# Performance work log

Measured on AMD Instinct MI355X. Metric: run time of the kernel, lower is better.

The kernel has to match this reference:

```python
import jax, jax.numpy as jnp
import numpy as np

D = 1024
H = 16
HD = D // H
LN_EPS = 1e-5
RMS_EPS = 1e-6


def layernorm(x, g, b):
    mu = jnp.mean(x, axis=-1, keepdims=True)
    var = jnp.mean(jnp.square(x - mu), axis=-1, keepdims=True)
    return (x - mu) * jax.lax.rsqrt(var + LN_EPS) * g + b


def rmsnorm(x, w):
    ms = jnp.mean(jnp.square(x), axis=-1, keepdims=True)
    return x * jax.lax.rsqrt(ms + RMS_EPS) * w


def setup_inputs() -> dict:
    key = jax.random.key(0)
    ks = jax.random.split(key, 8)
    s = 0.02
    ones = jnp.ones((D,), jnp.float32)
    zeros = jnp.zeros((D,), jnp.float32)
    return {
        "query_tokens": jax.random.normal(ks[0], (4, 512, D), jnp.float32),
        "point_features": jax.random.normal(ks[1], (4, 4096, D), jnp.float32),
        "ln_q_g": ones, "ln_q_b": zeros,
        "ln_kv_g": ones, "ln_kv_b": zeros,
        "Wq": jax.random.normal(ks[2], (D, D), jnp.float32) * s, "bq": zeros,
        "Wk": jax.random.normal(ks[3], (D, D), jnp.float32) * s, "bk": zeros,
        "Wv": jax.random.normal(ks[4], (D, D), jnp.float32) * s, "bv": zeros,
        "rms_q_w": ones, "rms_k_w": ones,
        "Wo": jax.random.normal(ks[5], (D, D), jnp.float32) * s, "bo": zeros,
        "ln_mlp_g": ones, "ln_mlp_b": zeros,
        "W1": jax.random.normal(ks[6], (D, 4 * D), jnp.float32) * s,
        "b1": jnp.zeros((4 * D,), jnp.float32),
        "W2": jax.random.normal(ks[7], (4 * D, D), jnp.float32) * s,
        "b2": zeros,
    }


def reference(query_tokens, point_features, ln_q_g, ln_q_b, ln_kv_g, ln_kv_b,
              Wq, bq, Wk, bk, Wv, bv, rms_q_w, rms_k_w, Wo, bo,
              ln_mlp_g, ln_mlp_b, W1, b1, W2, b2):
    B, K, _ = query_tokens.shape
    N = point_features.shape[1]
    q_in = layernorm(query_tokens, ln_q_g, ln_q_b)
    kv_in = layernorm(point_features, ln_kv_g, ln_kv_b)
    q = rmsnorm(q_in @ Wq + bq, rms_q_w)          # [B,K,D]
    k = rmsnorm(kv_in @ Wk + bk, rms_k_w)         # [B,N,D]
    v = kv_in @ Wv + bv                            # [B,N,D]
    q = q.reshape(B, K, H, HD)
    k = k.reshape(B, N, H, HD)
    v = v.reshape(B, N, H, HD)
    scores = jnp.einsum('bkhd,bnhd->bhkn', q, k) / jnp.sqrt(jnp.float32(HD))
    attn = jax.nn.softmax(scores, axis=-1)
    ctx = jnp.einsum('bhkn,bnhd->bkhd', attn, v).reshape(B, K, D)
    out = ctx @ Wo + bo + query_tokens
    h = layernorm(out, ln_mlp_g, ln_mlp_b)
    mlp = jax.nn.gelu(h @ W1 + b1, approximate=False) @ W2 + b2
    return out + mlp
```

## Files before the change

kernel.cpp:

```cpp
#include <hip/hip_runtime.h>
#include <math.h>

#define DD   1024
#define NHD  16
#define HDIM 64
#define BB   4
#define QN   512
#define KVN  4096
#define FF   4096

typedef __attribute__((ext_vector_type(8))) short bf16x8;
typedef __attribute__((ext_vector_type(4))) float f32x4;

__device__ __forceinline__ float b2f(ushort u){
  union { unsigned u32; float f; } x; x.u32 = ((unsigned)u)<<16; return x.f;
}
__device__ __forceinline__ ushort f2b(float f){
  unsigned u = __float_as_uint(f);
  unsigned r = (u + 0x7FFFu + ((u>>16)&1u)) >> 16;
  return (ushort)r;
}
__device__ __forceinline__ float ldx(const void* p, size_t i, int isbf){
  return isbf ? b2f(((const ushort*)p)[i]) : ((const float*)p)[i];
}
__device__ __forceinline__ int detect_bf(const void* gref){
  return ((const unsigned*)gref)[0] == 0x3F803F80u;
}

#if defined(__has_builtin)
#if __has_builtin(__builtin_amdgcn_global_load_lds)
#define HAS_GLL 1
#endif
#endif
#ifndef HAS_GLL
#define HAS_GLL 0
#endif
__device__ __forceinline__ void stage16(const ushort* g, ushort* lds_base, int lane){
#if HAS_GLL
  __builtin_amdgcn_global_load_lds(g, lds_base, 16, 0, 0);
#else
  *(uint4*)(lds_base + lane*8) = *(const uint4*)g;
#endif
}

__device__ __forceinline__ void wave_barrier(){
  asm volatile("" ::: "memory");
  __builtin_amdgcn_s_barrier();
  asm volatile("" ::: "memory");
}

__global__ __launch_bounds__(256)
void trans_all(const void* __restrict__ Wq, const void* __restrict__ Wk,
               const void* __restrict__ Wv, const void* __restrict__ Wo,
               const void* __restrict__ W1, const void* __restrict__ W2,
               ushort* __restrict__ WqT, ushort* __restrict__ WkvT,
               ushort* __restrict__ WoT,
               ushort* __restrict__ W1T, ushort* __restrict__ W2T,
               const void* __restrict__ gref)
{
  const int isbf = detect_bf(gref);
  int bid = blockIdx.x;
  const void* src; ushort* dst; int R, C, tid;
  if (bid < 1024){
    int s = bid >> 8; tid = bid & 255; R = 1024; C = 1024;
    src = (s==0) ? Wq : (s==1) ? Wk : (s==2) ? Wv : Wo;
    dst = (s==0) ? WqT : (s==1) ? WkvT : (s==2) ? (WkvT + (size_t)1024*1024) : WoT;
  } else if (bid < 2048){ tid = bid - 1024; src = W1; dst = W1T; R = 1024; C = 4096; }
  else                  { tid = bid - 2048; src = W2; dst = W2T; R = 4096; C = 1024; }
  int ntx = C >> 6;
  int tx = tid % ntx, ty = tid / ntx;
  int r0 = ty*64, c0 = tx*64;

  __shared__ __align__(16) ushort tile[64][72];
  int t = threadIdx.x;
  if (isbf){
    #pragma unroll
    for (int i=0;i<2;i++){
      int idx = t + i*256;
      int r = idx>>3, ch = idx&7;
      #pragma unroll
      for (int j=0;j<8;j++)
        tile[r][ch*8+j] = ((const ushort*)src)[(size_t)(r0+r)*C + c0 + ch*8 + j];
    }
  } else {
    #pragma unroll
    for (int i=0;i<2;i++){
      int idx = t + i*256;
      int r = idx>>3, ch = idx&7;
      const float* s4 = (const float*)src + (size_t)(r0+r)*C + c0 + ch*8;
      float4 f0 = *(const float4*)s4;
      float4 f1 = *(const float4*)(s4+4);
      tile[r][ch*8+0]=f2b(f0.x); tile[r][ch*8+1]=f2b(f0.y);
      tile[r][ch*8+2]=f2b(f0.z); tile[r][ch*8+3]=f2b(f0.w);
      tile[r][ch*8+4]=f2b(f1.x); tile[r][ch*8+5]=f2b(f1.y);
      tile[r][ch*8+6]=f2b(f1.z); tile[r][ch*8+7]=f2b(f1.w);
    }
  }
  __syncthreads();
  #pragma unroll
  for (int i=0;i<2;i++){
    int idx = t + i*256;
    int c = idx>>3, ch = idx&7;
    __align__(16) ushort tmp[8];
    #pragma unroll
    for (int j=0;j<8;j++) tmp[j] = tile[ch*8+j][c];
    *(uint4*)(dst + (size_t)(c0+c)*R + r0 + ch*8) = *(uint4*)tmp;
  }
}

__global__ __launch_bounds__(256)
void ln_all(const void* __restrict__ qtok, const void* __restrict__ pfeat,
            const void* __restrict__ gq, const void* __restrict__ bq,
            const void* __restrict__ gkv, const void* __restrict__ bkv,
            ushort* __restrict__ q_ln, ushort* __restrict__ kv_ln,
            const void* __restrict__ gref)
{
  const int isbf = detect_bf(gref);
  int row = blockIdx.x, t = threadIdx.x;
  const void* src; const void* g; const void* bb; ushort* dst; int r;
  if (row < BB*QN){ src = qtok;  g = gq;  bb = bq;  dst = q_ln;  r = row; }
  else            { src = pfeat; g = gkv; bb = bkv; dst = kv_ln; r = row - BB*QN; }
  int c0 = t*4;
  float v[4];
  if (isbf){
    #pragma unroll
    for (int i=0;i<4;i++) v[i] = b2f(((const ushort*)src)[(size_t)r*DD + c0 + i]);
  } else {
    float4 f = *(const float4*)((const float*)src + (size_t)r*DD + c0);
    v[0]=f.x; v[1]=f.y; v[2]=f.z; v[3]=f.w;
  }
  float s1=0.f, s2=0.f;
  #pragma unroll
  for (int i=0;i<4;i++){ s1 += v[i]; s2 += v[i]*v[i]; }
  #pragma unroll
  for (int off=32; off; off>>=1){ s1 += __shfl_xor(s1,off,64); s2 += __shfl_xor(s2,off,64); }
  __shared__ float r1[4], r2[4];
  int wave = t>>6;
  if ((t&63)==0){ r1[wave]=s1; r2[wave]=s2; }
  __syncthreads();
  s1 = r1[0]+r1[1]+r1[2]+r1[3];
  s2 = r2[0]+r2[1]+r2[2]+r2[3];
  float mu  = s1 * (1.0f/DD);
  float var = s2 * (1.0f/DD) - mu*mu;
  float rs  = rsqrtf(var + 1e-5f);
  union { ushort u[4]; uint2 w; } pk;
  #pragma unroll
  for (int i=0;i<4;i++)
    pk.u[i] = f2b((v[i]-mu)*rs*ldx(g,c0+i,isbf) + ldx(bb,c0+i,isbf));
  *(uint2*)(dst + (size_t)r*DD + c0) = pk.w;
}

__global__ __launch_bounds__(256)
void ln_f32(const float* __restrict__ x, const void* __restrict__ g,
            const void* __restrict__ bb, ushort* __restrict__ y,
            const void* __restrict__ gref)
{
  const int isbf = detect_bf(gref);
  int row = blockIdx.x, t = threadIdx.x;
  int c0 = t*4;
  float4 f = *(const float4*)(x + (size_t)row*DD + c0);
  float v[4] = {f.x, f.y, f.z, f.w};
  float s1=0.f, s2=0.f;
  #pragma unroll
  for (int i=0;i<4;i++){ s1 += v[i]; s2 += v[i]*v[i]; }
  #pragma unroll
  for (int off=32; off; off>>=1){ s1 += __shfl_xor(s1,off,64); s2 += __shfl_xor(s2,off,64); }
  __shared__ float r1[4], r2[4];
  int wave = t>>6;
  if ((t&63)==0){ r1[wave]=s1; r2[wave]=s2; }
  __syncthreads();
  s1 = r1[0]+r1[1]+r1[2]+r1[3];
  s2 = r2[0]+r2[1]+r2[2]+r2[3];
  float mu  = s1 * (1.0f/DD);
  float var = s2 * (1.0f/DD) - mu*mu;
  float rs  = rsqrtf(var + 1e-5f);
  union { ushort u[4]; uint2 w; } pk;
  #pragma unroll
  for (int i=0;i<4;i++)
    pk.u[i] = f2b((v[i]-mu)*rs*ldx(g,c0+i,isbf) + ldx(bb,c0+i,isbf));
  *(uint2*)(y + (size_t)row*DD + c0) = pk.w;
}

__global__ __launch_bounds__(256)
void rms_all(ushort* __restrict__ qb, const void* __restrict__ wq,
             ushort* __restrict__ kb, const void* __restrict__ wk,
             const void* __restrict__ gref)
{
  const int isbf = detect_bf(gref);
  int row = blockIdx.x, t = threadIdx.x;
  ushort* x; const void* w; int r;
  if (row < BB*QN){ x = qb; w = wq; r = row; }
  else            { x = kb; w = wk; r = row - BB*QN; }
  int c0 = t*4;
  union { ushort u[4]; uint2 w; } in;
  in.w = *(const uint2*)(x + (size_t)r*DD + c0);
  float v[4];
  #pragma unroll
  for (int i=0;i<4;i++) v[i] = b2f(in.u[i]);
  float s2 = 0.f;
  #pragma unroll
  for (int i=0;i<4;i++) s2 += v[i]*v[i];
  #pragma unroll
  for (int off=32; off; off>>=1) s2 += __shfl_xor(s2,off,64);
  __shared__ float r2[4];
  int wave = t>>6;
  if ((t&63)==0) r2[wave]=s2;
  __syncthreads();
  s2 = r2[0]+r2[1]+r2[2]+r2[3];
  float rs = rsqrtf(s2*(1.0f/DD) + 1e-6f);
  union { ushort u[4]; uint2 w; } pk;
  #pragma unroll
  for (int i=0;i<4;i++) pk.u[i] = f2b(v[i]*rs*ldx(w,c0+i,isbf));
  *(uint2*)(x + (size_t)r*DD + c0) = pk.w;
}

template<int ACT_GELU, int OUT_MODE, int RES_MODE>
__global__ __launch_bounds__(256)
void gemm_bt(const ushort* __restrict__ A, const ushort* __restrict__ BT,
             const void* __restrict__ bias,
             const void* __restrict__ res_ext, const float* __restrict__ res_f,
             void* __restrict__ Cout, void* __restrict__ Cout2,
             int M, int N, int Kdim,
             const void* __restrict__ gref)
{
  const int isbf = detect_bf(gref);
  __shared__ __align__(16) ushort As[128*64];
  __shared__ __align__(16) ushort Bs[128*64];
  const int bm = blockIdx.y * 128;
  const int bn = blockIdx.x * 128;
  const int t = threadIdx.x;
  const int wave = t>>6, lane = t&63, quad = lane>>4, l16 = lane&15;
  const int wm = (wave&1)*64, wn = (wave>>1)*64;

  const ushort* ga[4]; const ushort* gb[4];
  #pragma unroll
  for (int j=0;j<4;j++){
    int row = (t>>3) + j*32;
    int g = ((t&7) - row) & 7;
    ga[j] = A  + (size_t)(bm+row)*Kdim + g*8;
    gb[j] = BT + (size_t)(bn+row)*Kdim + g*8;
  }

  int offA[2][4], offB[2][4];
  #pragma unroll
  for (int kk=0;kk<2;kk++)
    #pragma unroll
    for (int i=0;i<4;i++){
      int ra = wm + i*16 + l16;
      offA[kk][i] = ra*64 + ((quad + kk*4 + ra)&7)*8;
      int rb = wn + i*16 + l16;
      offB[kk][i] = rb*64 + ((quad + kk*4 + rb)&7)*8;
    }

  f32x4 zero = {0.f,0.f,0.f,0.f};
  f32x4 acc[4][4];
  #pragma unroll
  for (int i=0;i<4;i++)
    #pragma unroll
    for (int j=0;j<4;j++) acc[i][j] = zero;

  const int kiters = Kdim >> 6;
  for (int ki = 0; ki < kiters; ki++) {
    #pragma unroll
    for (int j=0;j<4;j++){
      stage16(ga[j], As + (size_t)(j*256 + wave*64)*8, lane);
      stage16(gb[j], Bs + (size_t)(j*256 + wave*64)*8, lane);
      ga[j] += 64; gb[j] += 64;
    }
    __syncthreads();
    #pragma unroll
    for (int kk=0;kk<2;kk++){
      bf16x8 af[4], bfr[4];
      #pragma unroll
      for (int i=0;i<4;i++){
        af[i]  = *(const bf16x8*)(As + offA[kk][i]);
        bfr[i] = *(const bf16x8*)(Bs + offB[kk][i]);
      }
      #pragma unroll
      for (int mt=0;mt<4;mt++)
        #pragma unroll
        for (int nt=0;nt<4;nt++)
          acc[mt][nt] = __builtin_amdgcn_mfma_f32_16x16x32_bf16(af[mt], bfr[nt], acc[mt][nt], 0,0,0);
    }
    __syncthreads();
  }

  if (OUT_MODE == 3){
    if (bn < 1024){
      float bv[4];
      #pragma unroll
      for (int nt=0;nt<4;nt++) bv[nt] = ldx(bias, bn + wn + nt*16 + l16, isbf);
      ushort* kout = (ushort*)Cout;
      #pragma unroll
      for (int mt=0;mt<4;mt++){
        #pragma unroll
        for (int r=0;r<4;r++){
          int row = bm + wm + mt*16 + quad*4 + r;
          #pragma unroll
          for (int nt=0;nt<4;nt++){
            int col = bn + wn + nt*16 + l16;
            kout[(size_t)row*1024 + col] = f2b(acc[mt][nt][r] + bv[nt]);
          }
        }
      }
    } else {
      float bv[4];
      #pragma unroll
      for (int nt=0;nt<4;nt++) bv[nt] = ldx(res_ext, bn-1024 + wn + nt*16 + l16, isbf);
      ushort* Vt = (ushort*)Cout2;
      #pragma unroll
      for (int mt=0;mt<4;mt++){
        int row0 = bm + wm + mt*16 + quad*4;
        int b = row0 >> 12, tok = row0 & (KVN-1);
        #pragma unroll
        for (int nt=0;nt<4;nt++){
          int cl = bn-1024 + wn + nt*16 + l16;
          union { ushort u[4]; uint2 w; } pk;
          #pragma unroll
          for (int r=0;r<4;r++) pk.u[r] = f2b(acc[mt][nt][r] + bv[nt]);
          size_t o = ((size_t)((b*NHD + (cl>>6))*HDIM + (cl&63)))*KVN + tok;
          *(uint2*)(Vt + o) = pk.w;
        }
      }
    }
    return;
  }

  float bv[4];
  #pragma unroll
  for (int nt=0;nt<4;nt++) bv[nt] = ldx(bias, bn + wn + nt*16 + l16, isbf);
  #pragma unroll
  for (int mt=0;mt<4;mt++){
    #pragma unroll
    for (int r=0;r<4;r++){
      int row = bm + wm + mt*16 + quad*4 + r;
      #pragma unroll
      for (int nt=0;nt<4;nt++){
        int col = bn + wn + nt*16 + l16;
        float v = acc[mt][nt][r] + bv[nt];
        if (ACT_GELU) v = 0.5f*v*(1.0f + erff(v*0.70710678118f));
        size_t oi = (size_t)row*N + col;
        if (RES_MODE==1) v += ldx(res_ext, oi, isbf);
        if (RES_MODE==2) v += res_f[oi];
        if (OUT_MODE==0)      ((ushort*)Cout)[oi] = f2b(v);
        else if (OUT_MODE==1) ((float*)Cout)[oi]  = v;
        else { if (isbf) ((ushort*)Cout)[oi] = f2b(v); else ((float*)Cout)[oi] = v; }
      }
    }
  }
}

#define G_HB  32768
#define G_RA0 0
#define G_RA1 8192
#define G_RB0 16384
#define G_RB1 24576

#define G_STAGE(src, R, tile) do{ \
  ushort* _d = ldsb + (((tile)&1)*G_HB + (R) + wave*1024); \
  stage16(src[0] + ((tile)<<6), _d,       lane); \
  stage16(src[1] + ((tile)<<6), _d + 512, lane); \
}while(0)

#define G_LDA(dst, base) \
  _Pragma("unroll") for (int kk=0;kk<2;kk++) \
  _Pragma("unroll") for (int m=0;m<4;m++) \
    dst[kk][m] = *(const bf16x8*)((base) + offA[kk][m]);

#define G_LDB(dst, base) \
  _Pragma("unroll") for (int kk=0;kk<2;kk++) \
  _Pragma("unroll") for (int n=0;n<2;n++) \
    dst[kk][n] = *(const bf16x8*)((base) + offB[kk][n]);

#define G_MM16(ar, br, MO, NO) \
  _Pragma("unroll") for (int kk=0;kk<2;kk++) \
  _Pragma("unroll") for (int m=0;m<4;m++) \
  _Pragma("unroll") for (int n=0;n<2;n++) \
    acc[m+(MO)][n+(NO)] = __builtin_amdgcn_mfma_f32_16x16x32_bf16(ar[kk][m], br[kk][n], acc[m+(MO)][n+(NO)], 0,0,0);

#define G_SYNC() do{ wave_barrier(); \
  asm volatile("s_waitcnt lgkmcnt(0)" ::: "memory"); \
  __builtin_amdgcn_sched_barrier(0); \
  __builtin_amdgcn_s_setprio(1); }while(0)

#define G_END() do{ __builtin_amdgcn_s_setprio(0); wave_barrier(); }while(0)

__global__ __launch_bounds__(512, 2)
void gemm256_kv(const ushort* __restrict__ A, const ushort* __restrict__ BT,
                const void* __restrict__ biasK, const void* __restrict__ biasV,
                ushort* __restrict__ Kout, ushort* __restrict__ Vt,
                int Kdim, const void* __restrict__ gref)
{
  const int isbf = detect_bf(gref);
  __shared__ __align__(16) ushort ldsb[65536];
  const int bm = blockIdx.y * 256;
  const int bn = blockIdx.x * 256;
  const int t = threadIdx.x;
  const int wave = t>>6, lane = t&63, quad = lane>>4, l16 = lane&15;
  const int wg = wave>>2, wn = wave&3;

  const ushort *sA0[2], *sA1[2], *sB0[2], *sB1[2];
  #pragma unroll
  for (int jj=0;jj<2;jj++){
    int r = (wave*2 + jj)*8 + (lane>>3);
    int g = ((lane&7) - r) & 7;
    int grA0 = r + (r & 64);
    int gc0  = (r & 31) + ((r >> 5) << 6);
    sA0[jj] = A  + (size_t)(bm + grA0     )*Kdim + g*8;
    sA1[jj] = A  + (size_t)(bm + grA0 + 64)*Kdim + g*8;
    sB0[jj] = BT + (size_t)(bn + gc0      )*Kdim + g*8;
    sB1[jj] = BT + (size_t)(bn + gc0 + 32 )*Kdim + g*8;
  }

  int offA[2][4], offB[2][2];
  #pragma unroll
  for (int kk=0;kk<2;kk++){
    int slot = ((kk*4 + quad + l16) & 7) * 8;
    #pragma unroll
    for (int m=0;m<4;m++) offA[kk][m] = (wg*64 + m*16 + l16)*64 + slot;
    #pragma unroll
    for (int n=0;n<2;n++) offB[kk][n] = (wn*32 + n*16 + l16)*64 + slot;
  }

  f32x4 zero = {0.f,0.f,0.f,0.f};
  f32x4 acc[8][4];
  #pragma unroll
  for (int i=0;i<8;i++)
    #pragma unroll
    for (int j=0;j<4;j++) acc[i][j] = zero;

  G_STAGE(sA0, G_RA0, 0);
  G_STAGE(sB0, G_RB0, 0);
  G_STAGE(sB1, G_RB1, 0);
  G_STAGE(sA1, G_RA1, 0);
  G_STAGE(sA0, G_RA0, 1);
  G_STAGE(sB1, G_RB1, 1);
  G_STAGE(sA1, G_RA1, 1);
  asm volatile("s_waitcnt vmcnt(6)" ::: "memory");
  wave_barrier();

  const int niter = Kdim >> 7;
  const ushort* L0 = ldsb;
  const ushort* L1 = ldsb + G_HB;
  bf16x8 a[2][4], b[2][2], b1[2][2];

  for (int i = 0; i < niter; ++i) {
    const bool st = (i + 1 < niter);
    G_LDA(a, L0 + G_RA0); G_LDB(b, L0 + G_RB0);
    G_STAGE(sB0, G_RB0, 2*i+1);
    G_SYNC(); G_MM16(a, b, 0, 0); G_END();
    G_LDB(b1, L0 + G_RB1);
    if (st) G_STAGE(sA0, G_RA0, 2*i+2);
    G_SYNC(); G_MM16(a, b1, 0, 2); G_END();
    G_LDA(a, L0 + G_RA1);
    if (st) G_STAGE(sB1, G_RB1, 2*i+2);
    G_SYNC(); G_MM16(a, b1, 4, 2); G_END();
    G_LDB(b, L0 + G_RB0);
    if (st) G_STAGE(sA1, G_RA1, 2*i+2);
    G_SYNC(); G_MM16(a, b, 4, 0);
    __builtin_amdgcn_s_setprio(0);
    if (st) { asm volatile("s_waitcnt vmcnt(6)" ::: "memory"); }
    else    { asm volatile("s_waitcnt vmcnt(0)" ::: "memory"); }
    wave_barrier();
    G_LDA(a, L1 + G_RA0); G_LDB(b, L1 + G_RB0);
    if (st) G_STAGE(sB0, G_RB0, 2*i+2);
    G_SYNC(); G_MM16(a, b, 0, 0); G_END();
    G_LDB(b1, L1 + G_RB1);
    if (st) G_STAGE(sA0, G_RA0, 2*i+3);
    G_SYNC(); G_MM16(a, b1, 0, 2); G_END();
    G_LDA(a, L1 + G_RA1);
    if (st) G_STAGE(sB1, G_RB1, 2*i+3);
    G_SYNC(); G_MM16(a, b1, 4, 2); G_END();
    G_LDB(b, L1 + G_RB0);
    if (st) G_STAGE(sA1, G_RA1, 2*i+3);
    G_SYNC(); G_MM16(a, b, 4, 0);
    __builtin_amdgcn_s_setprio(0);
    if (st) { asm volatile("s_waitcnt vmcnt(6)" ::: "memory"); }
    wave_barrier();
  }

  if (bn < 1024){
    float bvv[4];
    #pragma unroll
    for (int nt=0;nt<4;nt++) bvv[nt] = ldx(biasK, bn + wn*64 + nt*16 + l16, isbf);
    #pragma unroll
    for (int mt=0;mt<8;mt++){
      #pragma unroll
      for (int r=0;r<4;r++){
        int row = bm + wg*128 + mt*16 + quad*4 + r;
        #pragma unroll
        for (int nt=0;nt<4;nt++){
          int col = bn + wn*64 + nt*16 + l16;
          Kout[(size_t)row*1024 + col] = f2b(acc[mt][nt][r] + bvv[nt]);
        }
      }
    }
  } else {
    float bvv[4];
    #pragma unroll
    for (int nt=0;nt<4;nt++) bvv[nt] = ldx(biasV, bn - 1024 + wn*64 + nt*16 + l16, isbf);
    #pragma unroll
    for (int mt=0;mt<8;mt++){
      int row0 = bm + wg*128 + mt*16 + quad*4;
      int bi = row0 >> 12, tok = row0 & (KVN-1);
      #pragma unroll
      for (int nt=0;nt<4;nt++){
        int cl = bn - 1024 + wn*64 + nt*16 + l16;
        union { ushort u[4]; uint2 w2; } pk;
        #pragma unroll
        for (int r=0;r<4;r++) pk.u[r] = f2b(acc[mt][nt][r] + bvv[nt]);
        size_t o = ((size_t)((bi*NHD + (cl>>6))*HDIM + (cl&63)))*KVN + tok;
        *(uint2*)(Vt + o) = pk.w2;
      }
    }
  }
}

__global__ __launch_bounds__(256, 3)
void flash_attn3(const ushort* __restrict__ Q, const ushort* __restrict__ K,
                 const ushort* __restrict__ Vt, float* __restrict__ Op,
                 float* __restrict__ ML)
{
  __shared__ __align__(16) ushort Ks[128*72];
  __shared__ __align__(16) ushort Vs[64*136];
  __shared__ __align__(16) ushort Ps[4][16*136];
  const int bh = blockIdx.x, qt = blockIdx.y, hf = blockIdx.z;
  const int b = bh>>4, h = bh&15;
  const int t = threadIdx.x, wave = t>>6, lane = t&63, quad = lane>>4, l16 = lane&15;
  ushort* Pz = Ps[wave];

  const float QS = 0.125f * 1.4426950408889634f;
  bf16x8 qf[2][2];
  #pragma unroll
  for (int mt=0;mt<2;mt++){
    const ushort* qb = Q + (size_t)(b*QN + qt*128 + wave*32 + mt*16 + l16)*DD + h*HDIM;
    bf16x8 r0 = *(const bf16x8*)(qb + quad*8);
    bf16x8 r1 = *(const bf16x8*)(qb + 32 + quad*8);
    #pragma unroll
    for (int j=0;j<8;j++){
      qf[mt][0][j] = (short)f2b(b2f((ushort)r0[j]) * QS);
      qf[mt][1][j] = (short)f2b(b2f((ushort)r1[j]) * QS);
    }
  }

  f32x4 zero = {0.f,0.f,0.f,0.f};
  f32x4 o[2][4];
  #pragma unroll
  for (int mt=0;mt<2;mt++)
    #pragma unroll
    for (int nt=0;nt<4;nt++) o[mt][nt] = zero;
  float lp[2][4] = {{0.f,0.f,0.f,0.f},{0.f,0.f,0.f,0.f}};

  const ushort* kgb = K  + (size_t)(b*KVN + hf*1024)*DD + h*HDIM;
  const ushort* vtb = Vt + ((size_t)bh*HDIM)*KVN + hf*1024;
  const int kcs = t&7;

  for (int kv0 = 0; kv0 < 1024; kv0 += 128) {
    #pragma unroll
    for (int j=0;j<4;j++){
      int kr = (t>>3) + j*32;
      *(uint4*)(Ks + kr*72 + kcs*8) =
        *(const uint4*)(kgb + (size_t)(kv0+kr)*DD + kcs*8);
    }
    #pragma unroll
    for (int j=0;j<4;j++){
      int p = t + j*256; int vr = p>>4, vc = p&15;
      uint4 d = *(const uint4*)(vtb + (size_t)vr*KVN + kv0 + vc*8);
      ushort* pv = (ushort*)&d;
      ushort* vbp = Vs + vr*136 + (vc&1)*64 + (vc>>1);
      #pragma unroll
      for (int jj=0;jj<8;jj++) vbp[jj*8] = pv[jj];
    }
    __syncthreads();

    f32x4 pb[2][8];
    #pragma unroll
    for (int nt=0;nt<8;nt++){
      const ushort* kb = Ks + (nt*16+l16)*72 + quad*8;
      bf16x8 kf0 = *(const bf16x8*)kb;
      bf16x8 kf1 = *(const bf16x8*)(kb + 32);
      #pragma unroll
      for (int mt=0;mt<2;mt++){
        f32x4 a = __builtin_amdgcn_mfma_f32_16x16x32_bf16(qf[mt][0], kf0, zero, 0,0,0);
        a = __builtin_amdgcn_mfma_f32_16x16x32_bf16(qf[mt][1], kf1, a, 0,0,0);
        #pragma unroll
        for (int r=0;r<4;r++) a[r] = __builtin_amdgcn_exp2f(fminf(a[r], 88.f));
        pb[mt][nt] = a;
      }
    }
    #pragma unroll
    for (int mt=0;mt<2;mt++){
      #pragma unroll
      for (int r=0;r<4;r++){
        float ls = 0.f;
        bf16x8 pk;
        #pragma unroll
        for (int nt=0;nt<8;nt++){
          ls += pb[mt][nt][r];
          pk[nt] = (short)(__float_as_uint(pb[mt][nt][r]) >> 16);
        }
        lp[mt][r] += ls;
        *(bf16x8*)(Pz + (quad*4+r)*136 + l16*8) = pk;
      }
      #pragma unroll
      for (int kc=0;kc<4;kc++){
        bf16x8 pa = *(const bf16x8*)(Pz + l16*136 + kc*32 + quad*8);
        pb[mt][kc] = *(f32x4*)&pa;
      }
    }
    #pragma unroll
    for (int nt=0;nt<4;nt++){
      const ushort* vbr = Vs + (nt*16+l16)*136;
      #pragma unroll
      for (int kc=0;kc<4;kc++){
        bf16x8 vf = *(const bf16x8*)(vbr + kc*32 + quad*8);
        o[0][nt] = __builtin_amdgcn_mfma_f32_16x16x32_bf16(*(bf16x8*)&pb[0][kc], vf, o[0][nt], 0,0,0);
        o[1][nt] = __builtin_amdgcn_mfma_f32_16x16x32_bf16(*(bf16x8*)&pb[1][kc], vf, o[1][nt], 0,0,0);
      }
    }
    __syncthreads();
  }

  const int slot = hf*256 + bh*4 + qt;
  float* Ob = Op + (size_t)slot*128*64;
  #pragma unroll
  for (int mt=0;mt<2;mt++)
    #pragma unroll
    for (int nt=0;nt<4;nt++)
      #pragma unroll
      for (int r=0;r<4;r++)
        Ob[(wave*32 + mt*16 + quad*4 + r)*64 + nt*16 + l16] = o[mt][nt][r];
  #pragma unroll
  for (int mt=0;mt<2;mt++)
    #pragma unroll
    for (int r=0;r<4;r++){
      float v = lp[mt][r];
      #pragma unroll
      for (int off=1; off<16; off<<=1) v += __shfl_xor(v, off, 64);
      if (l16 == 0)
        ML[(size_t)slot*128 + wave*32 + mt*16 + quad*4 + r] = v;
    }
}

__global__ __launch_bounds__(256)
void flash_combine4(const float* __restrict__ Op, const float* __restrict__ ML,
                    ushort* __restrict__ Ctx)
{
  const int bq = blockIdx.x;
  const int bh = bq>>2, qt = bq&3;
  const int b = bh>>4, h = bh&15;
  const int t = threadIdx.x;
  const int row = t>>1, hd0 = (t&1)*32;
  float l = 0.f;
  #pragma unroll
  for (int i=0;i<4;i++) l += ML[(size_t)(i*256 + bq)*128 + row];
  float inv = 1.0f / l;
  float4 a[8];
  #pragma unroll
  for (int c=0;c<8;c++){ a[c].x=0.f; a[c].y=0.f; a[c].z=0.f; a[c].w=0.f; }
  #pragma unroll
  for (int i=0;i<4;i++){
    const float* s = Op + ((size_t)(i*256 + bq)*128 + row)*64 + hd0;
    #pragma unroll
    for (int c=0;c<8;c++){
      float4 v = *(const float4*)(s + c*4);
      a[c].x += v.x; a[c].y += v.y; a[c].z += v.z; a[c].w += v.w;
    }
  }
  ushort* dst = Ctx + (size_t)(b*QN + qt*128 + row)*DD + h*HDIM + hd0;
  #pragma unroll
  for (int c=0;c<8;c++){
    union { ushort u[4]; uint2 w; } pk;
    pk.u[0] = f2b(a[c].x*inv); pk.u[1] = f2b(a[c].y*inv);
    pk.u[2] = f2b(a[c].z*inv); pk.u[3] = f2b(a[c].w*inv);
    *(uint2*)(dst + c*4) = pk.w;
  }
}

extern "C" void kernel_launch(void* const* d_in, const int* in_sizes, int n_in,
                              void* d_out, int out_size, void* d_ws, size_t ws_size,
                              hipStream_t stream)
{
  const void* qtok    = d_in[0];
  const void* pfeat   = d_in[1];
  const void* ln_q_g  = d_in[2];
  const void* ln_q_b  = d_in[3];
  const void* ln_kv_g = d_in[4];
  const void* ln_kv_b = d_in[5];
  const void* Wq      = d_in[6];
  const void* bq      = d_in[7];
  const void* Wk      = d_in[8];
  const void* bk      = d_in[9];
  const void* Wv      = d_in[10];
  const void* bv      = d_in[11];
  const void* rms_q_w = d_in[12];
  const void* rms_k_w = d_in[13];
  const void* Wo      = d_in[14];
  const void* bo      = d_in[15];
  const void* ln_mlp_g= d_in[16];
  const void* ln_mlp_b= d_in[17];
  const void* W1      = d_in[18];
  const void* b1      = d_in[19];
  const void* W2      = d_in[20];
  const void* b2      = d_in[21];
  const void* gref    = ln_q_g;

  char* w = (char*)d_ws;
  auto take = [&](size_t bytes)->char*{ char* p = w; w += (bytes + 255) & ~(size_t)255; return p; };
  ushort* WqT  = (ushort*)take((size_t)DD*DD*2);
  ushort* WkvT = (ushort*)take((size_t)2*DD*DD*2);
  ushort* WoT  = (ushort*)take((size_t)DD*DD*2);
  ushort* W1T  = (ushort*)take((size_t)DD*FF*2);
  ushort* W2T  = (ushort*)take((size_t)FF*DD*2);
  ushort* kv_ln= (ushort*)take((size_t)BB*KVN*DD*2);
  ushort* q_ln = (ushort*)take((size_t)BB*QN*DD*2);
  ushort* kbuf = (ushort*)take((size_t)BB*KVN*DD*2);
  ushort* qbuf = (ushort*)take((size_t)BB*QN*DD*2);
  ushort* Vt   = (ushort*)take((size_t)BB*KVN*DD*2);
  ushort* ctx  = WqT;
  float*  outb = (float*)kbuf;
  ushort* mlp1 = kv_ln;
  ushort* h_ln = q_ln;
  float*  Op   = (float*)kv_ln;
  float*  ML   = (float*)q_ln;

  trans_all<<<3072,256,0,stream>>>(Wq,Wk,Wv,Wo,W1,W2, WqT,WkvT,WoT,W1T,W2T, gref);
  ln_all<<<BB*QN + BB*KVN,256,0,stream>>>(qtok,pfeat, ln_q_g,ln_q_b, ln_kv_g,ln_kv_b,
                                          q_ln, kv_ln, gref);
  gemm_bt<0,0,0><<<dim3(8,16), 256,0,stream>>>(q_ln,  WqT, bq, nullptr,nullptr,
                                               qbuf, nullptr, BB*QN, DD, DD, gref);
  gemm256_kv<<<dim3(2*DD/256, BB*KVN/256), 512, 0, stream>>>(kv_ln, WkvT, bk, bv,
                                                             kbuf, Vt, DD, gref);
  rms_all<<<BB*QN + BB*KVN,256,0,stream>>>(qbuf, rms_q_w, kbuf, rms_k_w, gref);
  flash_attn3<<<dim3(64,4,4),256,0,stream>>>(qbuf, kbuf, Vt, Op, ML);
  flash_combine4<<<256,256,0,stream>>>(Op, ML, ctx);
  gemm_bt<0,1,1><<<dim3(8,16),256,0,stream>>>(ctx, WoT, bo, qtok, nullptr,
                                              outb, nullptr, BB*QN, DD, DD, gref);
  ln_f32<<<BB*QN,256,0,stream>>>(outb, ln_mlp_g, ln_mlp_b, h_ln, gref);
  gemm_bt<1,0,0><<<dim3(32,16),256,0,stream>>>(h_ln, W1T, b1, nullptr,nullptr,
                                               mlp1, nullptr, BB*QN, FF, DD, gref);
  gemm_bt<0,2,2><<<dim3(8,16), 256,0,stream>>>(mlp1, W2T, b2, nullptr, outb,
                                               d_out, nullptr, BB*QN, DD, FF, gref);
}
```

Measured before the change: 577.1 us.

## Split-K the Wo and W2 GEMMs and fuse partial reduction into epilogues

The Wo projection GEMM is split 2 ways along K and the W2 GEMM 4 ways, each writing fp32 partial tiles. This turns 128-block grids into 256 and 512 blocks so more CUs are busy. Bias, residual and the partial sum are folded into a new LayerNorm-combine kernel and a separate W2 combine kernel. A redundant LDS reload of the B fragment in the KV GEMM loop is also removed. The cost is extra fp32 partial-buffer traffic and one more kernel launch.

```diff
diff --git a/kernel.cpp b/kernel.cpp
--- a/kernel.cpp
+++ b/kernel.cpp
@@ -151,15 +151,33 @@
 }
 
 __global__ __launch_bounds__(256)
-void ln_f32(const float* __restrict__ x, const void* __restrict__ g,
-            const void* __restrict__ bb, ushort* __restrict__ y,
-            const void* __restrict__ gref)
+void ln_combine(const float* __restrict__ p0, const float* __restrict__ p1,
+                const void* __restrict__ bo, const void* __restrict__ qtok,
+                const void* __restrict__ g, const void* __restrict__ bb,
+                float* __restrict__ outb, ushort* __restrict__ y,
+                const void* __restrict__ gref)
 {
   const int isbf = detect_bf(gref);
   int row = blockIdx.x, t = threadIdx.x;
   int c0 = t*4;
-  float4 f = *(const float4*)(x + (size_t)row*DD + c0);
-  float v[4] = {f.x, f.y, f.z, f.w};
+  size_t base = (size_t)row*DD + c0;
+  float4 a0 = *(const float4*)(p0 + base);
+  float4 a1 = *(const float4*)(p1 + base);
+  float v[4] = {a0.x+a1.x, a0.y+a1.y, a0.z+a1.z, a0.w+a1.w};
+  if (isbf){
+    #pragma unroll
+    for (int i=0;i<4;i++)
+      v[i] += b2f(((const ushort*)qtok)[base+i]) + b2f(((const ushort*)bo)[c0+i]);
+  } else {
+    float4 q4 = *(const float4*)((const float*)qtok + base);
+    v[0] += q4.x + ((const float*)bo)[c0+0];
+    v[1] += q4.y + ((const float*)bo)[c0+1];
+    v[2] += q4.z + ((const float*)bo)[c0+2];
+    v[3] += q4.w + ((const float*)bo)[c0+3];
+  }
+  float4 ov; ov.x=v[0]; ov.y=v[1]; ov.z=v[2]; ov.w=v[3];
+  *(float4*)(outb + base) = ov;
+
   float s1=0.f, s2=0.f;
   #pragma unroll
   for (int i=0;i<4;i++){ s1 += v[i]; s2 += v[i]*v[i]; }
@@ -178,7 +196,35 @@
   #pragma unroll
   for (int i=0;i<4;i++)
     pk.u[i] = f2b((v[i]-mu)*rs*ldx(g,c0+i,isbf) + ldx(bb,c0+i,isbf));
-  *(uint2*)(y + (size_t)row*DD + c0) = pk.w;
+  *(uint2*)(y + base) = pk.w;
+}
+
+__global__ __launch_bounds__(256)
+void combine_w2(const float* __restrict__ parts, const void* __restrict__ b2,
+                const float* __restrict__ res, void* __restrict__ out,
+                const void* __restrict__ gref)
+{
+  const int isbf = detect_bf(gref);
+  size_t i = ((size_t)blockIdx.x*256 + threadIdx.x)*4;
+  float4 v = *(const float4*)(parts + i);
+  #pragma unroll
+  for (int z=1; z<4; z++){
+    float4 p = *(const float4*)(parts + (size_t)z*BB*QN*DD + i);
+    v.x+=p.x; v.y+=p.y; v.z+=p.z; v.w+=p.w;
+  }
+  float4 r = *(const float4*)(res + i);
+  int col = (int)(i & (DD-1));
+  v.x += r.x + ldx(b2,col+0,isbf);
+  v.y += r.y + ldx(b2,col+1,isbf);
+  v.z += r.z + ldx(b2,col+2,isbf);
+  v.w += r.w + ldx(b2,col+3,isbf);
+  if (isbf){
+    union { ushort u[4]; uint2 w; } pk;
+    pk.u[0]=f2b(v.x); pk.u[1]=f2b(v.y); pk.u[2]=f2b(v.z); pk.u[3]=f2b(v.w);
+    *(uint2*)((ushort*)out + i) = pk.w;
+  } else {
+    *(float4*)((float*)out + i) = v;
+  }
 }
 
 __global__ __launch_bounds__(256)
@@ -220,7 +266,7 @@
              const void* __restrict__ bias,
              const void* __restrict__ res_ext, const float* __restrict__ res_f,
              void* __restrict__ Cout, void* __restrict__ Cout2,
-             int M, int N, int Kdim,
+             int M, int N, int Kdim, int Kstride,
              const void* __restrict__ gref)
 {
   const int isbf = detect_bf(gref);
@@ -228,6 +274,7 @@
   __shared__ __align__(16) ushort Bs[128*64];
   const int bm = blockIdx.y * 128;
   const int bn = blockIdx.x * 128;
+  const int kz = blockIdx.z;
   const int t = threadIdx.x;
   const int wave = t>>6, lane = t&63, quad = lane>>4, l16 = lane&15;
   const int wm = (wave&1)*64, wn = (wave>>1)*64;
@@ -237,8 +284,8 @@
   for (int j=0;j<4;j++){
     int row = (t>>3) + j*32;
     int g = ((t&7) - row) & 7;
-    ga[j] = A  + (size_t)(bm+row)*Kdim + g*8;
-    gb[j] = BT + (size_t)(bn+row)*Kdim + g*8;
+    ga[j] = A  + (size_t)(bm+row)*Kstride + kz*Kdim + g*8;
+    gb[j] = BT + (size_t)(bn+row)*Kstride + kz*Kdim + g*8;
   }
 
   int offA[2][4], offB[2][4];
@@ -283,6 +330,23 @@
           acc[mt][nt] = __builtin_amdgcn_mfma_f32_16x16x32_bf16(af[mt], bfr[nt], acc[mt][nt], 0,0,0);
     }
     __syncthreads();
+  }
+
+  if (OUT_MODE == 4){
+    float* P = (float*)Cout + (size_t)kz*M*N;
+    #pragma unroll
+    for (int mt=0;mt<4;mt++){
+      #pragma unroll
+      for (int r=0;r<4;r++){
+        int row = bm + wm + mt*16 + quad*4 + r;
+        #pragma unroll
+        for (int nt=0;nt<4;nt++){
+          int col = bn + wn + nt*16 + l16;
+          P[(size_t)row*N + col] = acc[mt][nt][r];
+        }
+      }
+    }
+    return;
   }
 
   if (OUT_MODE == 3){
@@ -455,7 +519,6 @@
     G_LDA(a, L0 + G_RA1);
     if (st) G_STAGE(sB1, G_RB1, 2*i+2);
     G_SYNC(); G_MM16(a, b1, 4, 2); G_END();
-    G_LDB(b, L0 + G_RB0);
     if (st) G_STAGE(sA1, G_RA1, 2*i+2);
     G_SYNC(); G_MM16(a, b, 4, 0);
     __builtin_amdgcn_s_setprio(0);
@@ -471,7 +534,6 @@
     G_LDA(a, L1 + G_RA1);
     if (st) G_STAGE(sB1, G_RB1, 2*i+3);
     G_SYNC(); G_MM16(a, b1, 4, 2); G_END();
-    G_LDB(b, L1 + G_RB0);
     if (st) G_STAGE(sA1, G_RA1, 2*i+3);
     G_SYNC(); G_MM16(a, b, 4, 0);
     __builtin_amdgcn_s_setprio(0);
@@ -720,25 +782,29 @@
   ushort* ctx  = WqT;
   float*  outb = (float*)kbuf;
   ushort* mlp1 = kv_ln;
-  ushort* h_ln = q_ln;
   float*  Op   = (float*)kv_ln;
   float*  ML   = (float*)q_ln;
+  float*  o_parts  = (float*)kv_ln;
+  float*  w2_parts = (float*)Vt;
+  ushort* h_ln = q_ln;
 
   trans_all<<<3072,256,0,stream>>>(Wq,Wk,Wv,Wo,W1,W2, WqT,WkvT,WoT,W1T,W2T, gref);
   ln_all<<<BB*QN + BB*KVN,256,0,stream>>>(qtok,pfeat, ln_q_g,ln_q_b, ln_kv_g,ln_kv_b,
                                           q_ln, kv_ln, gref);
   gemm_bt<0,0,0><<<dim3(8,16), 256,0,stream>>>(q_ln,  WqT, bq, nullptr,nullptr,
-                                               qbuf, nullptr, BB*QN, DD, DD, gref);
+                                               qbuf, nullptr, BB*QN, DD, DD, DD, gref);
   gemm256_kv<<<dim3(2*DD/256, BB*KVN/256), 512, 0, stream>>>(kv_ln, WkvT, bk, bv,
                                                              kbuf, Vt, DD, gref);
   rms_all<<<BB*QN + BB*KVN,256,0,stream>>>(qbuf, rms_q_w, kbuf, rms_k_w, gref);
   flash_attn3<<<dim3(64,4,4),256,0,stream>>>(qbuf, kbuf, Vt, Op, ML);
   flash_combine4<<<256,256,0,stream>>>(Op, ML, ctx);
-  gemm_bt<0,1,1><<<dim3(8,16),256,0,stream>>>(ctx, WoT, bo, qtok, nullptr,
-                                              outb, nullptr, BB*QN, DD, DD, gref);
-  ln_f32<<<BB*QN,256,0,stream>>>(outb, ln_mlp_g, ln_mlp_b, h_ln, gref);
+  gemm_bt<0,4,0><<<dim3(8,16,2),256,0,stream>>>(ctx, WoT, nullptr, nullptr,nullptr,
+                                                o_parts, nullptr, BB*QN, DD, DD/2, DD, gref);
+  ln_combine<<<BB*QN,256,0,stream>>>(o_parts, o_parts + (size_t)BB*QN*DD,
+                                     bo, qtok, ln_mlp_g, ln_mlp_b, outb, h_ln, gref);
   gemm_bt<1,0,0><<<dim3(32,16),256,0,stream>>>(h_ln, W1T, b1, nullptr,nullptr,
-                                               mlp1, nullptr, BB*QN, FF, DD, gref);
-  gemm_bt<0,2,2><<<dim3(8,16), 256,0,stream>>>(mlp1, W2T, b2, nullptr, outb,
-                                               d_out, nullptr, BB*QN, DD, FF, gref);
-}
+                                               mlp1, nullptr, BB*QN, FF, DD, DD, gref);
+  gemm_bt<0,4,0><<<dim3(8,16,4),256,0,stream>>>(mlp1, W2T, nullptr, nullptr,nullptr,
+                                                w2_parts, nullptr, BB*QN, DD, FF/4, FF, gref);
+  combine_w2<<<BB*QN*DD/1024,256,0,stream>>>(w2_parts, b2, outb, d_out, gref);
+}
```

After: 521.8 us. 1.11x faster.
